# Performance work log

Hardware: AMD Instinct MI355X
Metric: run time of the kernel (lower is better)

Reference implementation:

```python
import jax, jax.numpy as jnp
import numpy as np

IN_DIM = 512
QK_DIM = IN_DIM // 8  # 64


def setup_inputs() -> dict:
    key = jax.random.key(0)
    ks = jax.random.split(key, 8)
    B, C, N = 16, IN_DIM, 2048
    s = 0.02
    return {
        "x": jax.random.normal(ks[0], (B, C, N), dtype=jnp.float32),
        "Wq": jax.random.normal(ks[1], (QK_DIM, C), dtype=jnp.float32) * s,
        "bq": jax.random.normal(ks[2], (QK_DIM,), dtype=jnp.float32) * s,
        "Wk": jax.random.normal(ks[3], (QK_DIM, C), dtype=jnp.float32) * s,
        "bk": jax.random.normal(ks[4], (QK_DIM,), dtype=jnp.float32) * s,
        "Wv": jax.random.normal(ks[5], (C, C), dtype=jnp.float32) * s,
        "bv": jax.random.normal(ks[6], (C,), dtype=jnp.float32) * s,
        "gamma": jax.random.normal(ks[7], (1,), dtype=jnp.float32) * 0.1,
    }


def reference(x, Wq, bq, Wk, bk, Wv, bv, gamma):
    # 1x1 conv == per-position linear over channels
    q = jnp.einsum("oc,bcn->bno", Wq, x) + bq          # [B, N, C/8] (permuted query)
    k = jnp.einsum("oc,bcn->bon", Wk, x) + bk[:, None]  # [B, C/8, N]
    energy = jnp.einsum("bno,bom->bnm", q, k)           # [B, N, N], no scaling (faithful)
    attention = jax.nn.softmax(energy, axis=-1)          # [B, N, N]
    v = jnp.einsum("oc,bcn->bon", Wv, x) + bv[:, None]  # [B, C, N]
    # out = bmm(value, attention^T): out[b,c,i] = sum_j v[b,c,j] * attention[b,i,j]
    out = jnp.einsum("bcj,bij->bci", v, attention)       # [B, C, N]
    return gamma * out + x
```

## Files before the change

kernel.cpp:

```cpp
#include <hip/hip_runtime.h>

#define B_ 16
#define C_ 512
#define N_ 2048
#define D_ 64

typedef unsigned short u16;
typedef unsigned int   u32;
typedef __bf16 bfv4 __attribute__((ext_vector_type(4)));
typedef __bf16 bfv8 __attribute__((ext_vector_type(8)));
typedef float  f4   __attribute__((ext_vector_type(4)));
typedef float  f16v __attribute__((ext_vector_type(16)));

__device__ __forceinline__ u16 f2bf(float f) {
  u32 u = __float_as_uint(f);
  u32 r = (u + 0x7FFFu + ((u >> 16) & 1u)) >> 16;
  return (u16)r;
}
__device__ __forceinline__ u32 pack2(float a, float b) {
  return (u32)f2bf(a) | ((u32)f2bf(b) << 16);
}
__device__ __forceinline__ bfv8 ld8(const u16* p) {
  bfv4 lo = *(const bfv4*)p;
  bfv4 hi = *(const bfv4*)(p + 4);
  bfv8 r;
  r[0] = lo[0]; r[1] = lo[1]; r[2] = lo[2]; r[3] = lo[3];
  r[4] = hi[0]; r[5] = hi[1]; r[6] = hi[2]; r[7] = hi[3];
  return r;
}

__global__ __launch_bounds__(256) void conv_all(
    const float* __restrict__ Wq, const float* __restrict__ Wk,
    const float* __restrict__ Wv,
    u16* __restrict__ Wqb, u16* __restrict__ Wkb, u16* __restrict__ Wvb) {
  const int q4 = D_ * C_ / 4;
  const int v4 = C_ * C_ / 4;
  int i = blockIdx.x * 256 + threadIdx.x;
  const float* src; u16* dst; int j;
  if (i < q4)            { src = Wq; dst = Wqb; j = i; }
  else if (i < 2 * q4)   { src = Wk; dst = Wkb; j = i - q4; }
  else                   { j = i - 2 * q4; if (j >= v4) return; src = Wv; dst = Wvb; }
  float4 v = ((const float4*)src)[j];
  ((uint2*)dst)[j] = make_uint2(pack2(v.x, v.y), pack2(v.z, v.w));
}

#define XS_STR 516
__global__ __launch_bounds__(256, 2) void proj_all(
    const float* __restrict__ x,
    const u16* __restrict__ Wqb, const u16* __restrict__ Wkb,
    const float* __restrict__ bq, const float* __restrict__ bk,
    const u16* __restrict__ Wvb, const float* __restrict__ bv,
    u16* __restrict__ Qb, u16* __restrict__ Kb, u16* __restrict__ Vb) {
  __shared__ u16 xs[64][XS_STR];
  const int b = blockIdx.x, n0 = blockIdx.y * 64;
  const int t = threadIdx.x;
  const int w = t >> 6, lane = t & 63;
  const int l15 = lane & 15, quad = lane >> 4;
  const int l31 = lane & 31, h = lane >> 5;

  {
    const int n4 = t & 15, cp = t >> 4;
#pragma unroll 2
    for (int p = 0; p < 16; p++) {
      int c = p * 32 + cp * 2;
      const size_t rb = ((size_t)(b * C_) + c) * N_ + n0 + n4 * 4;
      float4 a = *(const float4*)&x[rb];
      float4 bb = *(const float4*)&x[rb + N_];
      *(u32*)&xs[n4 * 4 + 0][c] = pack2(a.x, bb.x);
      *(u32*)&xs[n4 * 4 + 1][c] = pack2(a.y, bb.y);
      *(u32*)&xs[n4 * 4 + 2][c] = pack2(a.z, bb.z);
      *(u32*)&xs[n4 * 4 + 3][c] = pack2(a.w, bb.w);
    }
  }
  __syncthreads();

  {
    f4 accQ[4], accK[4];
#pragma unroll
    for (int nt = 0; nt < 4; nt++) { accQ[nt] = (f4)(0.0f); accK[nt] = (f4)(0.0f); }
    const u16* wqrow = &Wqb[(size_t)(w * 16 + l15) * C_];
    const u16* wkrow = &Wkb[(size_t)(w * 16 + l15) * C_];
    bfv8 aq = *(const bfv8*)&wqrow[quad * 8];
    bfv8 ak = *(const bfv8*)&wkrow[quad * 8];
    for (int kc = 0; kc < 16; kc++) {
      const int kn = (kc + 1) & 15;
      bfv8 aqn = *(const bfv8*)&wqrow[kn * 32 + quad * 8];
      bfv8 akn = *(const bfv8*)&wkrow[kn * 32 + quad * 8];
#pragma unroll
      for (int nt = 0; nt < 4; nt++) {
        bfv8 bx = ld8(&xs[nt * 16 + l15][kc * 32 + quad * 8]);
        accQ[nt] = __builtin_amdgcn_mfma_f32_16x16x32_bf16(aq, bx, accQ[nt], 0, 0, 0);
        accK[nt] = __builtin_amdgcn_mfma_f32_16x16x32_bf16(ak, bx, accK[nt], 0, 0, 0);
      }
      aq = aqn; ak = akn;
    }
    f4 bq4 = *(const f4*)&bq[w * 16 + quad * 4];
    f4 bk4 = *(const f4*)&bk[w * 16 + quad * 4];
#pragma unroll
    for (int nt = 0; nt < 4; nt++) {
      const size_t orow = ((size_t)(b * N_) + n0 + nt * 16 + l15) * D_ + w * 16 + quad * 4;
      *(uint2*)&Qb[orow] =
          make_uint2(pack2(accQ[nt][0] + bq4[0], accQ[nt][1] + bq4[1]),
                     pack2(accQ[nt][2] + bq4[2], accQ[nt][3] + bq4[3]));
      *(uint2*)&Kb[orow] =
          make_uint2(pack2(accK[nt][0] + bk4[0], accK[nt][1] + bk4[1]),
                     pack2(accK[nt][2] + bk4[2], accK[nt][3] + bk4[3]));
    }
  }

  {
    f16v acc[4][2];
#pragma unroll
    for (int mt = 0; mt < 4; mt++)
#pragma unroll
      for (int nt = 0; nt < 2; nt++) acc[mt][nt] = (f16v)(0.0f);
    const u16* wvrow[4];
#pragma unroll
    for (int mt = 0; mt < 4; mt++)
      wvrow[mt] = &Wvb[(size_t)(w * 128 + mt * 32 + l31) * C_ + h * 8];

    bfv8 acur[4], anxt[4];
#pragma unroll
    for (int mt = 0; mt < 4; mt++) acur[mt] = *(const bfv8*)&wvrow[mt][0];

    for (int kc2 = 0; kc2 < 16; kc2++) {
      {
        const int kc = 2 * kc2;
#pragma unroll
        for (int mt = 0; mt < 4; mt++)
          anxt[mt] = *(const bfv8*)&wvrow[mt][(kc + 1) * 16];
        bfv8 bx0 = ld8(&xs[l31][kc * 16 + h * 8]);
        bfv8 bx1 = ld8(&xs[32 + l31][kc * 16 + h * 8]);
#pragma unroll
        for (int mt = 0; mt < 4; mt++) {
          acc[mt][0] = __builtin_amdgcn_mfma_f32_32x32x16_bf16(acur[mt], bx0, acc[mt][0], 0, 0, 0);
          acc[mt][1] = __builtin_amdgcn_mfma_f32_32x32x16_bf16(acur[mt], bx1, acc[mt][1], 0, 0, 0);
        }
      }
      {
        const int kc = 2 * kc2 + 1;
        const int kn = (kc + 1) & 31;
#pragma unroll
        for (int mt = 0; mt < 4; mt++)
          acur[mt] = *(const bfv8*)&wvrow[mt][kn * 16];
        bfv8 bx0 = ld8(&xs[l31][kc * 16 + h * 8]);
        bfv8 bx1 = ld8(&xs[32 + l31][kc * 16 + h * 8]);
#pragma unroll
        for (int mt = 0; mt < 4; mt++) {
          acc[mt][0] = __builtin_amdgcn_mfma_f32_32x32x16_bf16(anxt[mt], bx0, acc[mt][0], 0, 0, 0);
          acc[mt][1] = __builtin_amdgcn_mfma_f32_32x32x16_bf16(anxt[mt], bx1, acc[mt][1], 0, 0, 0);
        }
      }
    }
#pragma unroll
    for (int mt = 0; mt < 4; mt++)
#pragma unroll
      for (int nt = 0; nt < 2; nt++)
#pragma unroll
        for (int g = 0; g < 4; g++) {
          f4 bv4 = *(const f4*)&bv[w * 128 + mt * 32 + g * 8 + h * 4];
#pragma unroll
          for (int r = 0; r < 4; r++) {
            int c = w * 128 + mt * 32 + g * 8 + h * 4 + r;
            Vb[((size_t)(b * C_) + c) * N_ + n0 + nt * 32 + l31] =
                f2bf(acc[mt][nt][g * 4 + r] + bv4[r]);
          }
        }
  }
}

#define PS_STR 68

__device__ __forceinline__ void stage_v(const u16* p0, u16* vsw, int j0) {
#pragma unroll
  for (int s = 0; s < 8; s++) {
    __builtin_amdgcn_global_load_lds(
        (const __attribute__((address_space(1))) void*)(p0 + (size_t)s * 8 * N_ + j0),
        (__attribute__((address_space(3))) void*)(vsw + s * 512),
        16, 0, 0);
  }
}

__global__ __launch_bounds__(256, 2) void attn(
    const float* __restrict__ x, const u16* __restrict__ Qb,
    const u16* __restrict__ Kb, const u16* __restrict__ Vb,
    const float* __restrict__ gamma, float* __restrict__ out) {
  __shared__ u16 Vs[4][64][64];
  __shared__ u16 Ps[2][128][PS_STR];
  __shared__ float invl[128];
  const int b = blockIdx.x, i0 = blockIdx.y * 128, ch = blockIdx.z;
  const int t = threadIdx.x, w = t >> 6, lane = t & 63;
  const int l15 = lane & 15, quad = lane >> 4;
  const int l31 = lane & 31, h = lane >> 5;

  const int sr = lane >> 3;
  const int sx = lane & 7;
  const int cbase = ch * 256 + w * 64;
  const u16* p0 = &Vb[((size_t)(b * C_) + cbase + sr) * N_ + ((sx ^ sr) << 3)];
  u16* vsw = &Vs[w][0][0];

  stage_v(p0, vsw, 0);

  bfv8 qf[2][2];
#pragma unroll
  for (int isub = 0; isub < 2; isub++)
#pragma unroll
    for (int kc = 0; kc < 2; kc++)
      qf[isub][kc] = *(const bfv8*)&Qb[((size_t)(b * N_) + i0 + w * 32 + isub * 16 + l15) * D_ +
                                       kc * 32 + quad * 8];

  f16v acc[4][2];
#pragma unroll
  for (int mt = 0; mt < 4; mt++)
#pragma unroll
    for (int nt = 0; nt < 2; nt++) acc[mt][nt] = (f16v)(0.0f);
  float la0 = 0.0f, la1 = 0.0f;
  const int swz = l31 & 7;

  int buf = 0;
  for (int j0 = 0; j0 < N_; j0 += 64, buf ^= 1) {
#pragma unroll
    for (int jt = 0; jt < 4; jt++) {
      const u16* krow = &Kb[((size_t)(b * N_) + j0 + jt * 16 + l15) * D_];
      bfv8 kf0 = *(const bfv8*)&krow[quad * 8];
      bfv8 kf1 = *(const bfv8*)&krow[32 + quad * 8];
      f4 e0 = (f4)(0.0f), e1 = (f4)(0.0f);
      e0 = __builtin_amdgcn_mfma_f32_16x16x32_bf16(kf0, qf[0][0], e0, 0, 0, 0);
      e0 = __builtin_amdgcn_mfma_f32_16x16x32_bf16(kf1, qf[0][1], e0, 0, 0, 0);
      e1 = __builtin_amdgcn_mfma_f32_16x16x32_bf16(kf0, qf[1][0], e1, 0, 0, 0);
      e1 = __builtin_amdgcn_mfma_f32_16x16x32_bf16(kf1, qf[1][1], e1, 0, 0, 0);
      {
        float p0_ = __expf(e0[0]), p1_ = __expf(e0[1]);
        float p2_ = __expf(e0[2]), p3_ = __expf(e0[3]);
        la0 += (p0_ + p1_) + (p2_ + p3_);
        *(uint2*)&Ps[buf][w * 32 + l15][jt * 16 + quad * 4] =
            make_uint2(pack2(p0_, p1_), pack2(p2_, p3_));
      }
      {
        float p0_ = __expf(e1[0]), p1_ = __expf(e1[1]);
        float p2_ = __expf(e1[2]), p3_ = __expf(e1[3]);
        la1 += (p0_ + p1_) + (p2_ + p3_);
        *(uint2*)&Ps[buf][w * 32 + 16 + l15][jt * 16 + quad * 4] =
            make_uint2(pack2(p0_, p1_), pack2(p2_, p3_));
      }
    }
    __syncthreads();

    __builtin_amdgcn_s_setprio(1);
#pragma unroll
    for (int kc = 0; kc < 4; kc++) {
      bfv8 pa[4];
#pragma unroll
      for (int mt = 0; mt < 4; mt++)
        pa[mt] = ld8(&Ps[buf][mt * 32 + l31][kc * 16 + h * 8]);
      bfv8 vb[2];
#pragma unroll
      for (int nt = 0; nt < 2; nt++)
        vb[nt] = *(const bfv8*)&vsw[(nt * 32 + l31) * 64 + (((kc * 2 + h) ^ swz) << 3)];
#pragma unroll
      for (int mt = 0; mt < 4; mt++)
#pragma unroll
        for (int nt = 0; nt < 2; nt++)
          acc[mt][nt] = __builtin_amdgcn_mfma_f32_32x32x16_bf16(pa[mt], vb[nt], acc[mt][nt], 0, 0, 0);
    }
    __builtin_amdgcn_s_setprio(0);
    __builtin_amdgcn_sched_barrier(0);
    if (j0 + 64 < N_) stage_v(p0, vsw, j0 + 64);
  }

  la0 += __shfl_xor(la0, 16, 64);
  la0 += __shfl_xor(la0, 32, 64);
  la1 += __shfl_xor(la1, 16, 64);
  la1 += __shfl_xor(la1, 32, 64);
  if (lane < 16) {
    invl[w * 32 + l15]      = 1.0f / la0;
    invl[w * 32 + 16 + l15] = 1.0f / la1;
  }
  __syncthreads();

  const float gam = gamma[0];
#pragma unroll
  for (int mt = 0; mt < 4; mt++)
#pragma unroll
    for (int nt = 0; nt < 2; nt++) {
      int c = cbase + nt * 32 + l31;
#pragma unroll
      for (int g = 0; g < 4; g++) {
        int ib = mt * 32 + g * 8 + h * 4;
        f4 il = *(const f4*)&invl[ib];
        size_t off = ((size_t)(b * C_) + c) * N_ + i0 + ib;
        f4 xv = *(const f4*)&x[off];
        f4 o;
#pragma unroll
        for (int r = 0; r < 4; r++)
          o[r] = xv[r] + gam * acc[mt][nt][g * 4 + r] * il[r];
        *(f4*)&out[off] = o;
      }
    }
}

extern "C" void kernel_launch(void* const* d_in, const int* in_sizes, int n_in,
                              void* d_out, int out_size, void* d_ws, size_t ws_size,
                              hipStream_t stream) {
  const float* x     = (const float*)d_in[0];
  const float* Wq    = (const float*)d_in[1];
  const float* bq    = (const float*)d_in[2];
  const float* Wk    = (const float*)d_in[3];
  const float* bk    = (const float*)d_in[4];
  const float* Wv    = (const float*)d_in[5];
  const float* bv    = (const float*)d_in[6];
  const float* gamma = (const float*)d_in[7];
  float* out = (float*)d_out;

  u16* wsu = (u16*)d_ws;
  u16* Qb  = wsu;
  u16* Kb  = Qb  + (size_t)B_ * N_ * D_;
  u16* Vb  = Kb  + (size_t)B_ * N_ * D_;
  u16* Wqb = Vb  + (size_t)B_ * C_ * N_;
  u16* Wkb = Wqb + (size_t)D_ * C_;
  u16* Wvb = Wkb + (size_t)D_ * C_;

  conv_all<<<dim3(320), 256, 0, stream>>>(Wq, Wk, Wv, Wqb, Wkb, Wvb);
  proj_all<<<dim3(B_, N_ / 64), 256, 0, stream>>>(x, Wqb, Wkb, bq, bk, Wvb, bv, Qb, Kb, Vb);
  attn<<<dim3(B_, N_ / 128, 2), 256, 0, stream>>>(x, Qb, Kb, Vb, gamma, out);
}
```

Before: 274.9 us.

## Split attention channels four ways with halved accumulators to raise occupancy

The attention kernel now splits channels across four z-blocks instead of two. Each wave pair shares a 64-channel V tile, and each wave accumulates only half of the 128 query rows, so accumulator registers and LDS use are halved and launch bounds rise to three blocks per CU. The P buffer is no longer double-buffered, so an extra __syncthreads per iteration guards reuse, and bf16 packing uses native conversion. In exchange, the QK^T and exp work is recomputed twice as often across the channel splits, and the added barrier cuts overlap.

```diff
diff --git a/kernel.cpp b/kernel.cpp
--- a/kernel.cpp
+++ b/kernel.cpp
@@ -171,35 +171,37 @@
 
 #define PS_STR 68
 
-__device__ __forceinline__ void stage_v(const u16* p0, u16* vsw, int j0) {
-#pragma unroll
-  for (int s = 0; s < 8; s++) {
+__device__ __forceinline__ void stage_v_half(const u16* p0, u16* vsw, int j0, int sh) {
+#pragma unroll
+  for (int s = 0; s < 4; s++) {
+    const int ss = sh + s;
     __builtin_amdgcn_global_load_lds(
-        (const __attribute__((address_space(1))) void*)(p0 + (size_t)s * 8 * N_ + j0),
-        (__attribute__((address_space(3))) void*)(vsw + s * 512),
+        (const __attribute__((address_space(1))) void*)(p0 + (size_t)ss * 8 * N_ + j0),
+        (__attribute__((address_space(3))) void*)(vsw + ss * 512),
         16, 0, 0);
   }
 }
 
-__global__ __launch_bounds__(256, 2) void attn(
+__global__ __launch_bounds__(256, 3) void attn(
     const float* __restrict__ x, const u16* __restrict__ Qb,
     const u16* __restrict__ Kb, const u16* __restrict__ Vb,
     const float* __restrict__ gamma, float* __restrict__ out) {
-  __shared__ u16 Vs[4][64][64];
-  __shared__ u16 Ps[2][128][PS_STR];
+  __shared__ u16 Vs[2][64][64];
+  __shared__ u16 Ps[128][PS_STR];
   __shared__ float invl[128];
   const int b = blockIdx.x, i0 = blockIdx.y * 128, ch = blockIdx.z;
   const int t = threadIdx.x, w = t >> 6, lane = t & 63;
   const int l15 = lane & 15, quad = lane >> 4;
   const int l31 = lane & 31, h = lane >> 5;
+  const int wp = w >> 1, wh = w & 1;
 
   const int sr = lane >> 3;
   const int sx = lane & 7;
-  const int cbase = ch * 256 + w * 64;
+  const int cbase = ch * 128 + wp * 64;
   const u16* p0 = &Vb[((size_t)(b * C_) + cbase + sr) * N_ + ((sx ^ sr) << 3)];
-  u16* vsw = &Vs[w][0][0];
-
-  stage_v(p0, vsw, 0);
+  u16* vsw = &Vs[wp][0][0];
+
+  stage_v_half(p0, vsw, 0, wh * 4);
 
   bfv8 qf[2][2];
 #pragma unroll
@@ -209,16 +211,15 @@
       qf[isub][kc] = *(const bfv8*)&Qb[((size_t)(b * N_) + i0 + w * 32 + isub * 16 + l15) * D_ +
                                        kc * 32 + quad * 8];
 
-  f16v acc[4][2];
-#pragma unroll
-  for (int mt = 0; mt < 4; mt++)
+  f16v acc[2][2];
+#pragma unroll
+  for (int mt = 0; mt < 2; mt++)
 #pragma unroll
     for (int nt = 0; nt < 2; nt++) acc[mt][nt] = (f16v)(0.0f);
   float la0 = 0.0f, la1 = 0.0f;
   const int swz = l31 & 7;
 
-  int buf = 0;
-  for (int j0 = 0; j0 < N_; j0 += 64, buf ^= 1) {
+  for (int j0 = 0; j0 < N_; j0 += 64) {
 #pragma unroll
     for (int jt = 0; jt < 4; jt++) {
       const u16* krow = &Kb[((size_t)(b * N_) + j0 + jt * 16 + l15) * D_];
@@ -233,15 +234,19 @@
         float p0_ = __expf(e0[0]), p1_ = __expf(e0[1]);
         float p2_ = __expf(e0[2]), p3_ = __expf(e0[3]);
         la0 += (p0_ + p1_) + (p2_ + p3_);
-        *(uint2*)&Ps[buf][w * 32 + l15][jt * 16 + quad * 4] =
-            make_uint2(pack2(p0_, p1_), pack2(p2_, p3_));
+        bfv4 pk;
+        pk[0] = (__bf16)p0_; pk[1] = (__bf16)p1_;
+        pk[2] = (__bf16)p2_; pk[3] = (__bf16)p3_;
+        *(bfv4*)&Ps[w * 32 + l15][jt * 16 + quad * 4] = pk;
       }
       {
         float p0_ = __expf(e1[0]), p1_ = __expf(e1[1]);
         float p2_ = __expf(e1[2]), p3_ = __expf(e1[3]);
         la1 += (p0_ + p1_) + (p2_ + p3_);
-        *(uint2*)&Ps[buf][w * 32 + 16 + l15][jt * 16 + quad * 4] =
-            make_uint2(pack2(p0_, p1_), pack2(p2_, p3_));
+        bfv4 pk;
+        pk[0] = (__bf16)p0_; pk[1] = (__bf16)p1_;
+        pk[2] = (__bf16)p2_; pk[3] = (__bf16)p3_;
+        *(bfv4*)&Ps[w * 32 + 16 + l15][jt * 16 + quad * 4] = pk;
       }
     }
     __syncthreads();
@@ -249,23 +254,23 @@
     __builtin_amdgcn_s_setprio(1);
 #pragma unroll
     for (int kc = 0; kc < 4; kc++) {
-      bfv8 pa[4];
-#pragma unroll
-      for (int mt = 0; mt < 4; mt++)
-        pa[mt] = ld8(&Ps[buf][mt * 32 + l31][kc * 16 + h * 8]);
+      bfv8 pa[2];
+#pragma unroll
+      for (int mt = 0; mt < 2; mt++)
+        pa[mt] = ld8(&Ps[wh * 64 + mt * 32 + l31][kc * 16 + h * 8]);
       bfv8 vb[2];
 #pragma unroll
       for (int nt = 0; nt < 2; nt++)
         vb[nt] = *(const bfv8*)&vsw[(nt * 32 + l31) * 64 + (((kc * 2 + h) ^ swz) << 3)];
 #pragma unroll
-      for (int mt = 0; mt < 4; mt++)
+      for (int mt = 0; mt < 2; mt++)
 #pragma unroll
         for (int nt = 0; nt < 2; nt++)
           acc[mt][nt] = __builtin_amdgcn_mfma_f32_32x32x16_bf16(pa[mt], vb[nt], acc[mt][nt], 0, 0, 0);
     }
     __builtin_amdgcn_s_setprio(0);
-    __builtin_amdgcn_sched_barrier(0);
-    if (j0 + 64 < N_) stage_v(p0, vsw, j0 + 64);
+    __syncthreads();
+    if (j0 + 64 < N_) stage_v_half(p0, vsw, j0 + 64, wh * 4);
   }
 
   la0 += __shfl_xor(la0, 16, 64);
@@ -280,13 +285,13 @@
 
   const float gam = gamma[0];
 #pragma unroll
-  for (int mt = 0; mt < 4; mt++)
+  for (int mt = 0; mt < 2; mt++)
 #pragma unroll
     for (int nt = 0; nt < 2; nt++) {
       int c = cbase + nt * 32 + l31;
 #pragma unroll
       for (int g = 0; g < 4; g++) {
-        int ib = mt * 32 + g * 8 + h * 4;
+        int ib = wh * 64 + mt * 32 + g * 8 + h * 4;
         f4 il = *(const f4*)&invl[ib];
         size_t off = ((size_t)(b * C_) + c) * N_ + i0 + ib;
         f4 xv = *(const f4*)&x[off];
@@ -322,5 +327,5 @@
 
   conv_all<<<dim3(320), 256, 0, stream>>>(Wq, Wk, Wv, Wqb, Wkb, Wvb);
   proj_all<<<dim3(B_, N_ / 64), 256, 0, stream>>>(x, Wqb, Wkb, bq, bk, Wvb, bv, Qb, Kb, Vb);
-  attn<<<dim3(B_, N_ / 128, 2), 256, 0, stream>>>(x, Qb, Kb, Vb, gamma, out);
-}
+  attn<<<dim3(B_, N_ / 128, 4), 256, 0, stream>>>(x, Qb, Kb, Vb, gamma, out);
+}
```

Measured after the change: 338.1 us. 23.0% more time.
